# Kernel optimization log

Hardware: AMD Instinct MI355X
Metric: run time of the kernel (lower is better)

The kernel has to match this reference:

```python
import jax, jax.numpy as jnp
import numpy as np

K = 10
ALPHA = 0.1
N_NODES = 100000
N_EDGES = 1000000
D_FEAT = 64


def setup_inputs() -> dict:
    key = jax.random.key(0)
    k1, k2, k3 = jax.random.split(key, 3)
    feat = jax.random.normal(k1, (N_NODES, D_FEAT), dtype=jnp.float32)
    edge_src = jax.random.randint(k2, (N_EDGES,), 0, N_NODES, dtype=jnp.int32)
    edge_dst = jax.random.randint(k3, (N_EDGES,), 0, N_NODES, dtype=jnp.int32)
    return {"feat": feat, "edge_src": edge_src, "edge_dst": edge_dst}


def reference(feat, edge_src, edge_dst):
    # APPNP: H^{t+1} = (1-alpha) * D^{-1/2} A D^{-1/2} H^t + alpha * H^0
    n = feat.shape[0]
    # in-degree per node (count of incoming edges), clamped to >= 1
    deg = jax.ops.segment_sum(
        jnp.ones_like(edge_dst, dtype=feat.dtype), edge_dst, num_segments=n
    )
    norm = jnp.power(jnp.clip(deg, 1.0, None), -0.5)[:, None]  # [N, 1]
    feat_0 = feat
    h = feat
    for _ in range(K):
        # message: neighbor feature scaled by neighbor norm
        msg = h[edge_src] * norm[edge_src]           # [E, D]
        agg = jax.ops.segment_sum(msg, edge_dst, num_segments=n)  # [N, D]
        h = (1.0 - ALPHA) * (agg * norm) + ALPHA * feat_0
    return h
```

## Files before the change

### kernel.cpp

```cpp
#include <hip/hip_runtime.h>
#include <hip/hip_bf16.h>
#include <hip/hip_fp16.h>


#define D_FEAT 64
#define K_ITERS 10
#define ALPHA 0.1f

#define SCAN_THREADS 4096
#define SCAN_BLOCKS  16

__global__ void count_deg_kernel(const int* __restrict__ dst, int* __restrict__ deg, int e) {
    int i = blockIdx.x * blockDim.x + threadIdx.x;
    if (i < e) atomicAdd(&deg[dst[i]], 1);
}

__global__ void partial_sum_kernel(const int* __restrict__ deg, int* __restrict__ tsums, int n) {
    int t = blockIdx.x * blockDim.x + threadIdx.x;
    int chunk = (n + SCAN_THREADS - 1) / SCAN_THREADS;
    int beg = t * chunk, end = min(beg + chunk, n);
    int s = 0;
    for (int i = beg; i < end; ++i) s += deg[i];
    tsums[t] = s;
}

__global__ void scan_partials_kernel(int* __restrict__ tsums) {
    __shared__ int part[1024];
    const int tid = threadIdx.x;
    int s0 = tsums[tid * 4 + 0], s1 = tsums[tid * 4 + 1];
    int s2 = tsums[tid * 4 + 2], s3 = tsums[tid * 4 + 3];
    int sum = s0 + s1 + s2 + s3;
    part[tid] = sum;
    __syncthreads();
    for (int off = 1; off < 1024; off <<= 1) {
        int t = (tid >= off) ? part[tid - off] : 0;
        __syncthreads();
        part[tid] += t;
        __syncthreads();
    }
    int ex = part[tid] - sum;
    tsums[tid * 4 + 0] = ex;
    tsums[tid * 4 + 1] = ex + s0;
    tsums[tid * 4 + 2] = ex + s0 + s1;
    tsums[tid * 4 + 3] = ex + s0 + s1 + s2;
}

__global__ void write_rowptr_kernel(const int* __restrict__ deg, const int* __restrict__ tsums,
                                    int* __restrict__ row_ptr, float* __restrict__ norm,
                                    int n, int e_total) {
    int t = blockIdx.x * blockDim.x + threadIdx.x;
    int chunk = (n + SCAN_THREADS - 1) / SCAN_THREADS;
    int beg = t * chunk, end = min(beg + chunk, n);
    int run = tsums[t];
    for (int i = beg; i < end; ++i) {
        row_ptr[i] = run;
        int d = deg[i];
        run += d;
        norm[i] = rsqrtf((float)max(d, 1));
    }
    if (t == 0) row_ptr[n] = e_total;
}

__global__ void bucket_kernel(const int* __restrict__ src, const int* __restrict__ dst,
                              const int* __restrict__ row_ptr, int* __restrict__ fill,
                              int* __restrict__ src_sorted, int e) {
    int i = blockIdx.x * blockDim.x + threadIdx.x;
    if (i < e) {
        int d = dst[i];
        int pos = row_ptr[d] + atomicAdd(&fill[d], 1);
        src_sorted[pos] = src[i];
    }
}

__global__ void f32_to_f16_kernel(const float* __restrict__ in, __half* __restrict__ out,
                                  int n4 ) {
    int i = blockIdx.x * blockDim.x + threadIdx.x;
    if (i < n4) {
        float4 v = reinterpret_cast<const float4*>(in)[i];
        __half2 a = __floats2half2_rn(v.x, v.y);
        __half2 b = __floats2half2_rn(v.z, v.w);
        uint2 o;
        o.x = *reinterpret_cast<unsigned int*>(&a);
        o.y = *reinterpret_cast<unsigned int*>(&b);
        reinterpret_cast<uint2*>(out)[i] = o;
    }
}

template<bool FINAL>
__global__ __launch_bounds__(256) void propagate_kernel(
        const __half* __restrict__ h, const float* __restrict__ feat0,
        const int* __restrict__ row_ptr, const int* __restrict__ src_sorted,
        const float* __restrict__ norm,
        __half* __restrict__ out_h, float* __restrict__ out_f, int n) {
    const int node = blockIdx.x * 4 + (threadIdx.x >> 6);
    if (node >= n) return;
    const int lane = threadIdx.x & 63;
    const int g   = lane >> 3;
    const int sub = lane & 7;

    const int beg = row_ptr[node];
    const int end = row_ptr[node + 1];

    float acc[8] = {0.f, 0.f, 0.f, 0.f, 0.f, 0.f, 0.f, 0.f};
    for (int e = beg + g; e < end; e += 8) {
        const int   s = src_sorted[e];
        const float w = norm[s];
        uint4 raw = *reinterpret_cast<const uint4*>(h + (size_t)s * D_FEAT + sub * 8);
        __half2 p0 = *reinterpret_cast<__half2*>(&raw.x);
        __half2 p1 = *reinterpret_cast<__half2*>(&raw.y);
        __half2 p2 = *reinterpret_cast<__half2*>(&raw.z);
        __half2 p3 = *reinterpret_cast<__half2*>(&raw.w);
        float2 f0 = __half22float2(p0), f1 = __half22float2(p1);
        float2 f2 = __half22float2(p2), f3 = __half22float2(p3);
        acc[0] += f0.x * w; acc[1] += f0.y * w;
        acc[2] += f1.x * w; acc[3] += f1.y * w;
        acc[4] += f2.x * w; acc[5] += f2.y * w;
        acc[6] += f3.x * w; acc[7] += f3.y * w;
    }

    #pragma unroll
    for (int off = 8; off <= 32; off <<= 1) {
        #pragma unroll
        for (int i = 0; i < 8; ++i) acc[i] += __shfl_xor(acc[i], off);
    }

    if (g == 0) {
        const float s = (1.0f - ALPHA) * norm[node];
        const size_t base = (size_t)node * D_FEAT + sub * 8;
        const float4 fa = *reinterpret_cast<const float4*>(feat0 + base);
        const float4 fb = *reinterpret_cast<const float4*>(feat0 + base + 4);
        float o[8];
        o[0] = s * acc[0] + ALPHA * fa.x;  o[1] = s * acc[1] + ALPHA * fa.y;
        o[2] = s * acc[2] + ALPHA * fa.z;  o[3] = s * acc[3] + ALPHA * fa.w;
        o[4] = s * acc[4] + ALPHA * fb.x;  o[5] = s * acc[5] + ALPHA * fb.y;
        o[6] = s * acc[6] + ALPHA * fb.z;  o[7] = s * acc[7] + ALPHA * fb.w;
        if (FINAL) {
            float4 w0 = make_float4(o[0], o[1], o[2], o[3]);
            float4 w1 = make_float4(o[4], o[5], o[6], o[7]);
            *reinterpret_cast<float4*>(out_f + base)     = w0;
            *reinterpret_cast<float4*>(out_f + base + 4) = w1;
        } else {
            __half2 h0 = __floats2half2_rn(o[0], o[1]);
            __half2 h1 = __floats2half2_rn(o[2], o[3]);
            __half2 h2 = __floats2half2_rn(o[4], o[5]);
            __half2 h3 = __floats2half2_rn(o[6], o[7]);
            uint4 w;
            w.x = *reinterpret_cast<unsigned int*>(&h0);
            w.y = *reinterpret_cast<unsigned int*>(&h1);
            w.z = *reinterpret_cast<unsigned int*>(&h2);
            w.w = *reinterpret_cast<unsigned int*>(&h3);
            *reinterpret_cast<uint4*>(out_h + base) = w;
        }
    }
}

static inline size_t align_up(size_t x, size_t a) { return (x + a - 1) & ~(a - 1); }

extern "C" void kernel_launch(void* const* d_in, const int* in_sizes, int n_in,
                              void* d_out, int out_size, void* d_ws, size_t ws_size,
                              hipStream_t stream) {
    const float* feat     = (const float*)d_in[0];
    const int*   edge_src = (const int*)d_in[1];
    const int*   edge_dst = (const int*)d_in[2];
    float*       out      = (float*)d_out;

    const int n = in_sizes[0] / D_FEAT;
    const int e = in_sizes[1];

    char* ws = (char*)d_ws;
    int*    deg        = (int*)ws;    ws += align_up((size_t)n * 4, 256);
    int*    row_ptr    = (int*)ws;    ws += align_up((size_t)(n + 1) * 4, 256);
    float*  norm       = (float*)ws;  ws += align_up((size_t)n * 4, 256);
    int*    fill       = (int*)ws;    ws += align_up((size_t)n * 4, 256);
    int*    tsums      = (int*)ws;    ws += align_up((size_t)SCAN_THREADS * 4, 256);
    int*    src_sorted = (int*)ws;    ws += align_up((size_t)e * 4, 256);
    __half* hA         = (__half*)ws; ws += align_up((size_t)n * D_FEAT * 2, 256);
    __half* hB         = (__half*)ws; ws += align_up((size_t)n * D_FEAT * 2, 256);

    hipMemsetAsync(deg,  0, (size_t)n * 4, stream);
    hipMemsetAsync(fill, 0, (size_t)n * 4, stream);

    const int eb = 256, eg = (e + eb - 1) / eb;
    count_deg_kernel<<<eg, eb, 0, stream>>>(edge_dst, deg, e);
    partial_sum_kernel<<<SCAN_BLOCKS, 256, 0, stream>>>(deg, tsums, n);
    scan_partials_kernel<<<1, 1024, 0, stream>>>(tsums);
    write_rowptr_kernel<<<SCAN_BLOCKS, 256, 0, stream>>>(deg, tsums, row_ptr, norm, n, e);
    bucket_kernel<<<eg, eb, 0, stream>>>(edge_src, edge_dst, row_ptr, fill, src_sorted, e);

    const int n4 = n * D_FEAT / 4;
    f32_to_f16_kernel<<<(n4 + 255) / 256, 256, 0, stream>>>(feat, hB, n4);

    const int pg = (n + 3) / 4;
    const __half* h_in = hB;
    for (int it = 1; it < K_ITERS; ++it) {
        __half* h_out = (it & 1) ? hA : hB;
        propagate_kernel<false><<<pg, 256, 0, stream>>>(h_in, feat, row_ptr, src_sorted,
                                                        norm, h_out, nullptr, n);
        h_in = h_out;
    }
    propagate_kernel<true><<<pg, 256, 0, stream>>>(h_in, feat, row_ptr, src_sorted,
                                                   norm, nullptr, out, n);
}
```

Measured before the change: 585.7 us.

## Propagate pre-normalized features to drop per-edge norm gather

Reformulates the iteration in terms of z = norm * h, so the inner edge loop no longer gathers norm[src] or multiplies per edge. A precomputed 0.9/deg factor and an fp16 seed z0 = norm*feat replace the fp32 feat0 read in intermediate iterations. The final iteration reconstructs h using norm and fp32 feat. It also splits bucketing into two launches and adds an extra fp16 buffer, with slightly different rounding because z0 is stored in fp16.

```diff
diff --git a/kernel.cpp b/kernel.cpp
--- a/kernel.cpp
+++ b/kernel.cpp
@@ -47,7 +47,7 @@
 
 __global__ void write_rowptr_kernel(const int* __restrict__ deg, const int* __restrict__ tsums,
                                     int* __restrict__ row_ptr, float* __restrict__ norm,
-                                    int n, int e_total) {
+                                    float* __restrict__ nsq, int n, int e_total) {
     int t = blockIdx.x * blockDim.x + threadIdx.x;
     int chunk = (n + SCAN_THREADS - 1) / SCAN_THREADS;
     int beg = t * chunk, end = min(beg + chunk, n);
@@ -56,42 +56,47 @@
         row_ptr[i] = run;
         int d = deg[i];
         run += d;
-        norm[i] = rsqrtf((float)max(d, 1));
+        float dc = (float)max(d, 1);
+        norm[i] = rsqrtf(dc);
+        nsq[i]  = 0.9f / dc;
     }
     if (t == 0) row_ptr[n] = e_total;
 }
 
 __global__ void bucket_kernel(const int* __restrict__ src, const int* __restrict__ dst,
                               const int* __restrict__ row_ptr, int* __restrict__ fill,
-                              int* __restrict__ src_sorted, int e) {
-    int i = blockIdx.x * blockDim.x + threadIdx.x;
-    if (i < e) {
+                              int* __restrict__ src_sorted, int e_beg, int e_end) {
+    int i = e_beg + blockIdx.x * blockDim.x + threadIdx.x;
+    if (i < e_end) {
         int d = dst[i];
         int pos = row_ptr[d] + atomicAdd(&fill[d], 1);
         src_sorted[pos] = src[i];
     }
 }
 
-__global__ void f32_to_f16_kernel(const float* __restrict__ in, __half* __restrict__ out,
-                                  int n4 ) {
+__global__ void seed_kernel(const float* __restrict__ feat, const float* __restrict__ norm,
+                            __half* __restrict__ z0, int n16 ) {
     int i = blockIdx.x * blockDim.x + threadIdx.x;
-    if (i < n4) {
-        float4 v = reinterpret_cast<const float4*>(in)[i];
-        __half2 a = __floats2half2_rn(v.x, v.y);
-        __half2 b = __floats2half2_rn(v.z, v.w);
+    if (i < n16) {
+        const int node = i >> 4;
+        const float nn = norm[node];
+        float4 v = reinterpret_cast<const float4*>(feat)[i];
+        __half2 a = __floats2half2_rn(v.x * nn, v.y * nn);
+        __half2 b = __floats2half2_rn(v.z * nn, v.w * nn);
         uint2 o;
         o.x = *reinterpret_cast<unsigned int*>(&a);
         o.y = *reinterpret_cast<unsigned int*>(&b);
-        reinterpret_cast<uint2*>(out)[i] = o;
+        reinterpret_cast<uint2*>(z0)[i] = o;
     }
 }
 
 template<bool FINAL>
 __global__ __launch_bounds__(256) void propagate_kernel(
-        const __half* __restrict__ h, const float* __restrict__ feat0,
+        const __half* __restrict__ z, const __half* __restrict__ z0,
+        const float* __restrict__ feat0,
         const int* __restrict__ row_ptr, const int* __restrict__ src_sorted,
-        const float* __restrict__ norm,
-        __half* __restrict__ out_h, float* __restrict__ out_f, int n) {
+        const float* __restrict__ norm, const float* __restrict__ nsq,
+        __half* __restrict__ out_z, float* __restrict__ out_f, int n) {
     const int node = blockIdx.x * 4 + (threadIdx.x >> 6);
     if (node >= n) return;
     const int lane = threadIdx.x & 63;
@@ -103,19 +108,18 @@
 
     float acc[8] = {0.f, 0.f, 0.f, 0.f, 0.f, 0.f, 0.f, 0.f};
     for (int e = beg + g; e < end; e += 8) {
-        const int   s = src_sorted[e];
-        const float w = norm[s];
-        uint4 raw = *reinterpret_cast<const uint4*>(h + (size_t)s * D_FEAT + sub * 8);
+        const int s = src_sorted[e];
+        uint4 raw = *reinterpret_cast<const uint4*>(z + (size_t)s * D_FEAT + sub * 8);
         __half2 p0 = *reinterpret_cast<__half2*>(&raw.x);
         __half2 p1 = *reinterpret_cast<__half2*>(&raw.y);
         __half2 p2 = *reinterpret_cast<__half2*>(&raw.z);
         __half2 p3 = *reinterpret_cast<__half2*>(&raw.w);
         float2 f0 = __half22float2(p0), f1 = __half22float2(p1);
         float2 f2 = __half22float2(p2), f3 = __half22float2(p3);
-        acc[0] += f0.x * w; acc[1] += f0.y * w;
-        acc[2] += f1.x * w; acc[3] += f1.y * w;
-        acc[4] += f2.x * w; acc[5] += f2.y * w;
-        acc[6] += f3.x * w; acc[7] += f3.y * w;
+        acc[0] += f0.x; acc[1] += f0.y;
+        acc[2] += f1.x; acc[3] += f1.y;
+        acc[4] += f2.x; acc[5] += f2.y;
+        acc[6] += f3.x; acc[7] += f3.y;
     }
 
     #pragma unroll
@@ -125,21 +129,32 @@
     }
 
     if (g == 0) {
-        const float s = (1.0f - ALPHA) * norm[node];
         const size_t base = (size_t)node * D_FEAT + sub * 8;
-        const float4 fa = *reinterpret_cast<const float4*>(feat0 + base);
-        const float4 fb = *reinterpret_cast<const float4*>(feat0 + base + 4);
-        float o[8];
-        o[0] = s * acc[0] + ALPHA * fa.x;  o[1] = s * acc[1] + ALPHA * fa.y;
-        o[2] = s * acc[2] + ALPHA * fa.z;  o[3] = s * acc[3] + ALPHA * fa.w;
-        o[4] = s * acc[4] + ALPHA * fb.x;  o[5] = s * acc[5] + ALPHA * fb.y;
-        o[6] = s * acc[6] + ALPHA * fb.z;  o[7] = s * acc[7] + ALPHA * fb.w;
         if (FINAL) {
-            float4 w0 = make_float4(o[0], o[1], o[2], o[3]);
-            float4 w1 = make_float4(o[4], o[5], o[6], o[7]);
+            const float s = 0.9f * norm[node];
+            const float4 fa = *reinterpret_cast<const float4*>(feat0 + base);
+            const float4 fb = *reinterpret_cast<const float4*>(feat0 + base + 4);
+            float4 w0, w1;
+            w0.x = s * acc[0] + ALPHA * fa.x;  w0.y = s * acc[1] + ALPHA * fa.y;
+            w0.z = s * acc[2] + ALPHA * fa.z;  w0.w = s * acc[3] + ALPHA * fa.w;
+            w1.x = s * acc[4] + ALPHA * fb.x;  w1.y = s * acc[5] + ALPHA * fb.y;
+            w1.z = s * acc[6] + ALPHA * fb.z;  w1.w = s * acc[7] + ALPHA * fb.w;
             *reinterpret_cast<float4*>(out_f + base)     = w0;
             *reinterpret_cast<float4*>(out_f + base + 4) = w1;
         } else {
+            const float s = nsq[node];
+            uint4 raw = *reinterpret_cast<const uint4*>(z0 + base);
+            __half2 q0 = *reinterpret_cast<__half2*>(&raw.x);
+            __half2 q1 = *reinterpret_cast<__half2*>(&raw.y);
+            __half2 q2 = *reinterpret_cast<__half2*>(&raw.z);
+            __half2 q3 = *reinterpret_cast<__half2*>(&raw.w);
+            float2 f0 = __half22float2(q0), f1 = __half22float2(q1);
+            float2 f2 = __half22float2(q2), f3 = __half22float2(q3);
+            float o[8];
+            o[0] = s * acc[0] + ALPHA * f0.x;  o[1] = s * acc[1] + ALPHA * f0.y;
+            o[2] = s * acc[2] + ALPHA * f1.x;  o[3] = s * acc[3] + ALPHA * f1.y;
+            o[4] = s * acc[4] + ALPHA * f2.x;  o[5] = s * acc[5] + ALPHA * f2.y;
+            o[6] = s * acc[6] + ALPHA * f3.x;  o[7] = s * acc[7] + ALPHA * f3.y;
             __half2 h0 = __floats2half2_rn(o[0], o[1]);
             __half2 h1 = __floats2half2_rn(o[2], o[3]);
             __half2 h2 = __floats2half2_rn(o[4], o[5]);
@@ -149,7 +164,7 @@
             w.y = *reinterpret_cast<unsigned int*>(&h1);
             w.z = *reinterpret_cast<unsigned int*>(&h2);
             w.w = *reinterpret_cast<unsigned int*>(&h3);
-            *reinterpret_cast<uint4*>(out_h + base) = w;
+            *reinterpret_cast<uint4*>(out_z + base) = w;
         }
     }
 }
@@ -171,33 +186,40 @@
     int*    deg        = (int*)ws;    ws += align_up((size_t)n * 4, 256);
     int*    row_ptr    = (int*)ws;    ws += align_up((size_t)(n + 1) * 4, 256);
     float*  norm       = (float*)ws;  ws += align_up((size_t)n * 4, 256);
+    float*  nsq        = (float*)ws;  ws += align_up((size_t)n * 4, 256);
     int*    fill       = (int*)ws;    ws += align_up((size_t)n * 4, 256);
     int*    tsums      = (int*)ws;    ws += align_up((size_t)SCAN_THREADS * 4, 256);
     int*    src_sorted = (int*)ws;    ws += align_up((size_t)e * 4, 256);
-    __half* hA         = (__half*)ws; ws += align_up((size_t)n * D_FEAT * 2, 256);
-    __half* hB         = (__half*)ws; ws += align_up((size_t)n * D_FEAT * 2, 256);
+    __half* z0         = (__half*)ws; ws += align_up((size_t)n * D_FEAT * 2, 256);
+    __half* zA         = (__half*)ws; ws += align_up((size_t)n * D_FEAT * 2, 256);
+    __half* zB         = (__half*)ws; ws += align_up((size_t)n * D_FEAT * 2, 256);
 
     hipMemsetAsync(deg,  0, (size_t)n * 4, stream);
     hipMemsetAsync(fill, 0, (size_t)n * 4, stream);
 
-    const int eb = 256, eg = (e + eb - 1) / eb;
-    count_deg_kernel<<<eg, eb, 0, stream>>>(edge_dst, deg, e);
+    const int eb = 256;
+    count_deg_kernel<<<(e + eb - 1) / eb, eb, 0, stream>>>(edge_dst, deg, e);
     partial_sum_kernel<<<SCAN_BLOCKS, 256, 0, stream>>>(deg, tsums, n);
     scan_partials_kernel<<<1, 1024, 0, stream>>>(tsums);
-    write_rowptr_kernel<<<SCAN_BLOCKS, 256, 0, stream>>>(deg, tsums, row_ptr, norm, n, e);
-    bucket_kernel<<<eg, eb, 0, stream>>>(edge_src, edge_dst, row_ptr, fill, src_sorted, e);
-
-    const int n4 = n * D_FEAT / 4;
-    f32_to_f16_kernel<<<(n4 + 255) / 256, 256, 0, stream>>>(feat, hB, n4);
+    write_rowptr_kernel<<<SCAN_BLOCKS, 256, 0, stream>>>(deg, tsums, row_ptr, norm, nsq, n, e);
+
+    const int eh = e / 2;
+    bucket_kernel<<<(eh + eb - 1) / eb, eb, 0, stream>>>(edge_src, edge_dst, row_ptr, fill,
+                                                         src_sorted, 0, eh);
+    bucket_kernel<<<(e - eh + eb - 1) / eb, eb, 0, stream>>>(edge_src, edge_dst, row_ptr, fill,
+                                                             src_sorted, eh, e);
+
+    const int n16 = n * D_FEAT / 4;
+    seed_kernel<<<(n16 + 255) / 256, 256, 0, stream>>>(feat, norm, z0, n16);
 
     const int pg = (n + 3) / 4;
-    const __half* h_in = hB;
+    const __half* z_in = z0;
     for (int it = 1; it < K_ITERS; ++it) {
-        __half* h_out = (it & 1) ? hA : hB;
-        propagate_kernel<false><<<pg, 256, 0, stream>>>(h_in, feat, row_ptr, src_sorted,
-                                                        norm, h_out, nullptr, n);
-        h_in = h_out;
-    }
-    propagate_kernel<true><<<pg, 256, 0, stream>>>(h_in, feat, row_ptr, src_sorted,
-                                                   norm, nullptr, out, n);
-}
+        __half* z_out = (it & 1) ? zA : zB;
+        propagate_kernel<false><<<pg, 256, 0, stream>>>(z_in, z0, nullptr, row_ptr, src_sorted,
+                                                        norm, nsq, z_out, nullptr, n);
+        z_in = z_out;
+    }
+    propagate_kernel<true><<<pg, 256, 0, stream>>>(z_in, z0, feat, row_ptr, src_sorted,
+                                                   norm, nsq, nullptr, out, n);
+}
```

After: 583.0 us. Within noise of the previous version (-0.5%).
